# Kernel optimization log

Hardware: AMD Instinct MI355X
Metric: run time of the kernel (lower is better)

## Reference

```python
import jax, jax.numpy as jnp
import numpy as np

B, L, D = 2, 1536, 1024
H, P = 16, 1024
HD = P // H  # 64
K_SIZE = 5
DIFF_STEPS = 3
ALPHA = 0.02
NEG = -1e9
EPS = 1e-9


def setup_inputs() -> dict:
    key = jax.random.key(0)
    ks = jax.random.split(key, 12)
    s = 0.02
    hidden_states = jax.random.normal(ks[0], (B, L, D), dtype=jnp.float32)
    attention_mask = jax.random.randint(ks[1], (B, L), 0, 2, dtype=jnp.int32)
    Wq = jax.random.normal(ks[2], (D, P), dtype=jnp.float32) * s
    bq = jax.random.normal(ks[3], (P,), dtype=jnp.float32) * s
    Wk = jax.random.normal(ks[4], (D, P), dtype=jnp.float32) * s
    bk = jax.random.normal(ks[5], (P,), dtype=jnp.float32) * s
    Wv = jax.random.normal(ks[6], (D, P), dtype=jnp.float32) * s
    bv = jax.random.normal(ks[7], (P,), dtype=jnp.float32) * s
    Wo = jax.random.normal(ks[8], (P, D), dtype=jnp.float32) * s
    bo = jax.random.normal(ks[9], (D,), dtype=jnp.float32) * s
    kernel_w = jax.random.normal(ks[10], (K_SIZE,), dtype=jnp.float32)
    return {"hidden_states": hidden_states, "attention_mask": attention_mask,
            "Wq": Wq, "bq": bq, "Wk": Wk, "bk": bk, "Wv": Wv, "bv": bv,
            "Wo": Wo, "bo": bo, "kernel_w": kernel_w}


def _causal_smooth(p, w):
    # p: (B,H,Lq,Lk); causal cross-correlation matching F.conv1d(pad=k-1)[:Lk]
    k = w.shape[0]
    Lk = p.shape[-1]
    pp = jnp.pad(p, ((0, 0), (0, 0), (0, 0), (k - 1, 0)))
    out = w[0] * pp[..., 0:Lk]
    for j in range(1, k):
        out = out + w[j] * pp[..., j:j + Lk]
    return out


def reference(hidden_states, attention_mask, Wq, bq, Wk, bk, Wv, bv, Wo, bo, kernel_w):
    mask_f = attention_mask.astype(hidden_states.dtype)  # (B,Lk), 1=keep
    additive = (1.0 - mask_f) * NEG                       # (B,Lk)
    key_valid = (attention_mask > 0).astype(hidden_states.dtype)

    Q = (hidden_states @ Wq + bq).reshape(B, L, H, HD)
    Kt = (hidden_states @ Wk + bk).reshape(B, L, H, HD)
    V = (hidden_states @ Wv + bv).reshape(B, L, H, HD)

    scores = jnp.einsum('bqhd,bkhd->bhqk', Q, Kt) / np.sqrt(HD).astype(np.float32)
    scores = scores + additive[:, None, None, :]
    p = jax.nn.softmax(scores, axis=-1)  # (B,H,Lq,Lk)

    w = jax.nn.softmax(kernel_w)  # (k,)
    kv4 = key_valid[:, None, None, :]
    for _ in range(DIFF_STEPS):
        ps = _causal_smooth(p, w)
        ps = ps * kv4
        ps = ps / (jnp.sum(ps, axis=-1, keepdims=True) + EPS)
        p = (1.0 - ALPHA) * p + ALPHA * ps

    attn = jnp.einsum('bhqk,bkhd->bqhd', p, V).reshape(B, L, P)
    return attn @ Wo + bo
```

## Files before the change

kernel.cpp:

```cpp
#include <hip/hip_runtime.h>

#define BB 2
#define LL 1536
#define DD 1024
#define HH 16
#define HDD 64
#define PP 1024
#define PBS 1544

typedef __attribute__((ext_vector_type(8))) __bf16 bf16x8;
typedef __attribute__((ext_vector_type(4))) float f32x4;
typedef __attribute__((ext_vector_type(2))) float f32x2;

__device__ __forceinline__ float b2f(unsigned short u) {
  unsigned int x = ((unsigned int)u) << 16;
  return __builtin_bit_cast(float, x);
}
__device__ __forceinline__ unsigned short f2b(float f) {
  unsigned int x = __builtin_bit_cast(unsigned int, f);
  unsigned int r = (x + 0x7FFFu + ((x >> 16) & 1u)) >> 16;
  return (unsigned short)r;
}
__device__ __forceinline__ bf16x8 ldb8(const unsigned short* p) {
  return __builtin_bit_cast(bf16x8, *(const uint4*)p);
}
__device__ __forceinline__ f32x2 mk2(float a, float b) {
  f32x2 r;
  r.x = a;
  r.y = b;
  return r;
}
__device__ __forceinline__ void gl_lds16(const unsigned short* g,
                                         unsigned short* l) {
  __builtin_amdgcn_global_load_lds(
      (const __attribute__((address_space(1))) void*)g,
      (__attribute__((address_space(3))) void*)l, 16, 0, 0);
}

template <int CTRL>
__device__ __forceinline__ float dppadd(float x) {
  int s = __builtin_amdgcn_update_dpp(0, __builtin_bit_cast(int, x), CTRL, 0xf,
                                      0xf, true);
  return x + __builtin_bit_cast(float, s);
}
__device__ __forceinline__ float wave_sum64(float x) {
  x = dppadd<0x111>(x);
  x = dppadd<0x112>(x);
  x = dppadd<0x114>(x);
  x = dppadd<0x118>(x);
  x = dppadd<0x142>(x);
  x = dppadd<0x143>(x);
  return __builtin_bit_cast(
      float, __builtin_amdgcn_readlane(__builtin_bit_cast(int, x), 63));
}

__global__ __launch_bounds__(256) void prep(
    const float* __restrict__ hs, unsigned short* __restrict__ hsb,
    const float* __restrict__ Wq, const float* __restrict__ Wk,
    const float* __restrict__ Wv, const float* __restrict__ Wo,
    unsigned short* __restrict__ WT) {
  const int bid = blockIdx.x;
  const int t = threadIdx.x;
  if (bid < 1536) {
    const int idx = bid * 2048 + t * 8;
    float4 a = *(const float4*)(hs + idx);
    float4 b = *(const float4*)(hs + idx + 4);
    uint4 u;
    u.x = (unsigned int)f2b(a.x) | ((unsigned int)f2b(a.y) << 16);
    u.y = (unsigned int)f2b(a.z) | ((unsigned int)f2b(a.w) << 16);
    u.z = (unsigned int)f2b(b.x) | ((unsigned int)f2b(b.y) << 16);
    u.w = (unsigned int)f2b(b.z) | ((unsigned int)f2b(b.w) << 16);
    *(uint4*)(hsb + idx) = u;
  } else {
    __shared__ float tile[64][68];
    const int t2 = bid - 1536;
    const int z = t2 >> 8;
    const int bx = t2 & 15, by = (t2 >> 4) & 15;
    const float* W = (z == 0) ? Wq : (z == 1) ? Wk : (z == 2) ? Wv : Wo;
    unsigned short* O = WT + (size_t)z * 1024 * 1024;
    const int r0 = by * 64;
    const int c0 = bx * 64;
#pragma unroll
    for (int i = 0; i < 4; ++i) {
      const int row = (t >> 4) + i * 16;
      const int col = (t & 15) * 4;
      *(float4*)&tile[row][col] =
          *(const float4*)&W[(size_t)(r0 + row) * 1024 + c0 + col];
    }
    __syncthreads();
#pragma unroll
    for (int i = 0; i < 4; ++i) {
      const int n = (t >> 4) + i * 16;
      const int k4 = (t & 15) * 4;
      uint2 u;
      u.x = (unsigned int)f2b(tile[k4 + 0][n]) |
            ((unsigned int)f2b(tile[k4 + 1][n]) << 16);
      u.y = (unsigned int)f2b(tile[k4 + 2][n]) |
            ((unsigned int)f2b(tile[k4 + 3][n]) << 16);
      *(uint2*)&O[(size_t)(c0 + n) * 1024 + r0 + k4] = u;
    }
  }
}

template <int MODE>
__device__ __forceinline__ void gemm_mfma_body(
    const unsigned short* __restrict__ A, const unsigned short* __restrict__ Bt,
    const float* __restrict__ bias, void* __restrict__ Cout) {
  __shared__ unsigned short As[128 * 32];
  __shared__ unsigned short Bs[128 * 32];
  const int t = threadIdx.x;
  const int lane = t & 63;
  const int w = t >> 6;
  const int quad = lane >> 4;
  const int lc = lane & 15;
  const int m0 = blockIdx.y * 128, n0 = blockIdx.x * 128;

  const int sr = lane >> 2;
  const int sk = (lane & 3) * 8;
  const unsigned short* ga0 = A + (size_t)(m0 + w * 32 + sr) * 1024 + sk;
  const unsigned short* ga1 = ga0 + 16 * 1024;
  const unsigned short* gb0 = Bt + (size_t)(n0 + w * 32 + sr) * 1024 + sk;
  const unsigned short* gb1 = gb0 + 16 * 1024;
  unsigned short* la0 = As + w * 1024;
  unsigned short* la1 = As + w * 1024 + 512;
  unsigned short* lb0 = Bs + w * 1024;
  unsigned short* lb1 = Bs + w * 1024 + 512;

  const int mrow0 = (w >> 1) * 64, ncol0 = (w & 1) * 64;

  f32x4 acc[4][4];
#pragma unroll
  for (int i = 0; i < 4; ++i)
#pragma unroll
    for (int j = 0; j < 4; ++j) acc[i][j] = (f32x4){0.f, 0.f, 0.f, 0.f};

  for (int k0 = 0; k0 < 1024; k0 += 32) {
    __syncthreads();
    gl_lds16(ga0 + k0, la0);
    gl_lds16(ga1 + k0, la1);
    gl_lds16(gb0 + k0, lb0);
    gl_lds16(gb1 + k0, lb1);
    __syncthreads();
    bf16x8 af[4], bfr[4];
#pragma unroll
    for (int i = 0; i < 4; ++i)
      af[i] = ldb8(&As[(mrow0 + i * 16 + lc) * 32 + quad * 8]);
#pragma unroll
    for (int j = 0; j < 4; ++j)
      bfr[j] = ldb8(&Bs[(ncol0 + j * 16 + lc) * 32 + quad * 8]);
#pragma unroll
    for (int i = 0; i < 4; ++i)
#pragma unroll
      for (int j = 0; j < 4; ++j)
        acc[i][j] =
            __builtin_amdgcn_mfma_f32_16x16x32_bf16(af[i], bfr[j], acc[i][j], 0, 0, 0);
  }

#pragma unroll
  for (int i = 0; i < 4; ++i) {
    const int row0 = m0 + mrow0 + i * 16 + quad * 4;
#pragma unroll
    for (int jj = 0; jj < 4; ++jj) {
      const int col = n0 + ncol0 + jj * 16 + lc;
      const float bz = bias[col];
      float o[4];
#pragma unroll
      for (int r = 0; r < 4; ++r) o[r] = acc[i][jj][r] + bz;
      if constexpr (MODE == 0) {
        const int bb = row0 / LL;
        const int ql = row0 - bb * LL;
        const int qt = ql >> 4;
        const int m = ql & 15;
        const int hh = col >> 6;
        const int hd = col & 63;
        const int f = hd >> 5;
        const int qk = (hd >> 3) & 3;
        const int j = hd & 7;
        unsigned short* QF = (unsigned short*)Cout;
        const size_t base =
            (((size_t)(bb * HH + hh) * 96 + qt) * 2 + f) * 512 +
            (qk * 16 + m) * 8 + j;
#pragma unroll
        for (int r = 0; r < 4; ++r) QF[base + r * 8] = f2b(o[r] * 0.125f);
      } else if constexpr (MODE == 1) {
        const int bb = row0 / LL;
        const int kl = row0 - bb * LL;
        const int ktl = kl >> 4;
        const int m = kl & 15;
        const int hh = col >> 6;
        const int hd = col & 63;
        const int f = hd >> 5;
        const int qk = (hd >> 3) & 3;
        const int j = hd & 7;
        unsigned short* KF = (unsigned short*)Cout;
        const size_t base =
            (((size_t)(bb * HH + hh) * 96 + ktl) * 2 + f) * 512 +
            (qk * 16 + m) * 8 + j;
#pragma unroll
        for (int r = 0; r < 4; ++r) KF[base + r * 8] = f2b(o[r]);
      } else if constexpr (MODE == 2) {
        const int bb = row0 / LL;
        const int kl = row0 - bb * LL;
        const int hh = col >> 6;
        const int hd = col & 63;
        const int hg = hd >> 4;
        const int lcv = hd & 15;
        const int tile = (kl >> 5);
        const int qv = (kl >> 3) & 3;
        const int j0 = kl & 7;
        unsigned short* VF = (unsigned short*)Cout;
        const size_t base =
            (((size_t)(bb * HH + hh) * 4 + hg) * 48 + tile) * 512 +
            (qv * 16 + lcv) * 8 + j0;
        uint2 u;
        u.x = (unsigned int)f2b(o[0]) | ((unsigned int)f2b(o[1]) << 16);
        u.y = (unsigned int)f2b(o[2]) | ((unsigned int)f2b(o[3]) << 16);
        *(uint2*)&VF[base] = u;
      } else {
#pragma unroll
        for (int r = 0; r < 4; ++r)
          ((float*)Cout)[(size_t)(row0 + r) * 1024 + col] = o[r];
      }
    }
  }
}

__global__ __launch_bounds__(256) void qkv_gemm(
    const unsigned short* __restrict__ hsb, const unsigned short* __restrict__ WT,
    const float* __restrict__ bq, const float* __restrict__ bk,
    const float* __restrict__ bv, unsigned short* __restrict__ QF,
    unsigned short* __restrict__ KF, unsigned short* __restrict__ VF) {
  if (blockIdx.z == 0) {
    gemm_mfma_body<0>(hsb, WT, bq, QF);
  } else if (blockIdx.z == 1) {
    gemm_mfma_body<1>(hsb, WT + 1024 * 1024, bk, KF);
  } else {
    gemm_mfma_body<2>(hsb, WT + 2 * 1024 * 1024, bv, VF);
  }
}

__global__ __launch_bounds__(256) void out_gemm(
    const unsigned short* __restrict__ ctxb,
    const unsigned short* __restrict__ WoT, const float* __restrict__ bo,
    float* __restrict__ out) {
  gemm_mfma_body<3>(ctxb, WoT, bo, out);
}

__global__ __launch_bounds__(512, 4) void attn_kernel(
    const unsigned short* __restrict__ QF, const unsigned short* __restrict__ KF,
    const unsigned short* __restrict__ VF, const int* __restrict__ mask,
    const float* __restrict__ kernel_w, unsigned short* __restrict__ ctxb) {
  __shared__ __align__(16) unsigned short p_b[16][PBS];
  __shared__ unsigned int kvb[50];
  __shared__ float red_s[8][16];

  const int t = threadIdx.x;
  const int lane = t & 63;
  const int w = t >> 6;
  const int quad = lane >> 4;
  const int lc = lane & 15;
  const int b = blockIdx.z, h = blockIdx.y;
  const int q0 = blockIdx.x * 16;

  if (t < 2) kvb[48 + t] = 0;
#pragma unroll
  for (int r = 0; r < 3; ++r) {
    const int idx = r * 512 + t;
    unsigned long long bal = __ballot(mask[b * LL + idx] > 0);
    if (lane == 0) {
      const int base = (r * 512 + w * 64) >> 5;
      kvb[base] = (unsigned int)bal;
      kvb[base + 1] = (unsigned int)(bal >> 32);
    }
  }
  __syncthreads();

  const unsigned short* qfb =
      QF + (((size_t)(b * HH + h) * 96 + (q0 >> 4)) * 2) * 512 + lane * 8;
  const bf16x8 qb0 = ldb8(qfb);
  const bf16x8 qb1 = ldb8(qfb + 512);
  float sc[12][4];
  const unsigned short* kfb =
      KF + (((size_t)(b * HH + h) * 96 + w) * 2) * 512 + lane * 8;
#pragma unroll
  for (int j = 0; j < 12; ++j) {
    bf16x8 ka0 = ldb8(kfb + j * 8192);
    bf16x8 ka1 = ldb8(kfb + j * 8192 + 512);
    f32x4 acc = {0.f, 0.f, 0.f, 0.f};
    acc = __builtin_amdgcn_mfma_f32_16x16x32_bf16(ka0, qb0, acc, 0, 0, 0);
    acc = __builtin_amdgcn_mfma_f32_16x16x32_bf16(ka1, qb1, acc, 0, 0, 0);
    sc[j][0] = acc[0];
    sc[j][1] = acc[1];
    sc[j][2] = acc[2];
    sc[j][3] = acc[3];
  }

  const int kbase = w * 16 + quad * 4;
  const int gamma = kbase >> 5;
  const int beta = kbase & 31;
  float s = 0.f;
#pragma unroll
  for (int j = 0; j < 12; ++j) {
    const unsigned int w4 = (kvb[j * 4 + gamma] >> beta) & 0xFu;
#pragma unroll
    for (int r = 0; r < 4; ++r) {
      float e = ((w4 >> r) & 1u) ? __expf(sc[j][r]) : 0.f;
      sc[j][r] = e;
      s += e;
    }
  }
  s += __shfl_xor(s, 16, 64);
  s += __shfl_xor(s, 32, 64);
  if (lane < 16) red_s[w][lane] = s;
  __syncthreads();
  float tot0 = 0.f;
#pragma unroll
  for (int ww = 0; ww < 8; ++ww) tot0 += red_s[ww][lc];
  const float inv = 1.f / tot0;
#pragma unroll
  for (int j = 0; j < 12; ++j) {
    uint2 u;
    u.x = (unsigned int)f2b(sc[j][0] * inv) |
          ((unsigned int)f2b(sc[j][1] * inv) << 16);
    u.y = (unsigned int)f2b(sc[j][2] * inv) |
          ((unsigned int)f2b(sc[j][3] * inv) << 16);
    *(uint2*)&p_b[lc][j * 128 + kbase] = u;
  }
  __syncthreads();

  float wr[5];
  {
    float k0 = kernel_w[0], k1 = kernel_w[1], k2 = kernel_w[2],
          k3 = kernel_w[3], k4 = kernel_w[4];
    float km = fmaxf(fmaxf(fmaxf(k0, k1), fmaxf(k2, k3)), k4);
    float e0 = __expf(k0 - km), e1 = __expf(k1 - km), e2 = __expf(k2 - km),
          e3 = __expf(k3 - km), e4 = __expf(k4 - km);
    float es = e0 + e1 + e2 + e3 + e4;
    wr[0] = e4 / es;
    wr[1] = e3 / es;
    wr[2] = e2 / es;
    wr[3] = e1 / es;
    wr[4] = e0 / es;
  }
  unsigned int db;
  {
    const int w0i = (lane * 24) >> 5, sh = (lane * 24) & 31;
    unsigned long long kw2 =
        ((unsigned long long)kvb[w0i + 1] << 32) | (unsigned long long)kvb[w0i];
    db = (unsigned int)((kw2 >> sh) & 0xFFFFFFu);
  }
  f32x2 fm2[12];
#pragma unroll
  for (int i = 0; i < 12; ++i)
    fm2[i] = mk2((float)((db >> (2 * i)) & 1u), (float)((db >> (2 * i + 1)) & 1u));

  for (int rr = 0; rr < 2; ++rr) {
    const int row = w * 2 + rr;
    f32x2 pg[12];
#pragma unroll
    for (int c = 0; c < 3; ++c) {
      uint4 v = *(const uint4*)&p_b[row][lane * 24 + c * 8];
      unsigned int ws4[4] = {v.x, v.y, v.z, v.w};
#pragma unroll
      for (int q = 0; q < 4; ++q)
        pg[c * 4 + q] =
            mk2(__builtin_bit_cast(float, ws4[q] << 16),
                __builtin_bit_cast(float, ws4[q] & 0xFFFF0000u));
    }
#pragma unroll
    for (int step = 0; step < 3; ++step) {
      float h1 = __shfl_up(pg[11].y, 1);
      float h2 = __shfl_up(pg[11].x, 1);
      float h3 = __shfl_up(pg[10].y, 1);
      float h4 = __shfl_up(pg[10].x, 1);
      if (lane == 0) h1 = h2 = h3 = h4 = 0.f;
      f32x2 ps2[12];
      ps2[0] = wr[0] * pg[0] + wr[1] * mk2(h1, pg[0].x) + wr[2] * mk2(h2, h1) +
               wr[3] * mk2(h3, h2) + wr[4] * mk2(h4, h3);
      ps2[1] = wr[0] * pg[1] + wr[1] * mk2(pg[0].y, pg[1].x) + wr[2] * pg[0] +
               wr[3] * mk2(h1, pg[0].x) + wr[4] * mk2(h2, h1);
#pragma unroll
      for (int i = 2; i < 12; ++i)
        ps2[i] = wr[0] * pg[i] + wr[1] * mk2(pg[i - 1].y, pg[i].x) +
                 wr[2] * pg[i - 1] + wr[3] * mk2(pg[i - 2].y, pg[i - 1].x) +
                 wr[4] * pg[i - 2];
      f32x2 acc2 = mk2(0.f, 0.f);
#pragma unroll
      for (int i = 0; i < 12; ++i) {
        ps2[i] *= fm2[i];
        acc2 += ps2[i];
      }
      const float tot = wave_sum64(acc2.x + acc2.y);
      const float pinv = 0.02f / (tot + 1e-9f);
#pragma unroll
      for (int i = 0; i < 12; ++i) pg[i] = 0.98f * pg[i] + ps2[i] * pinv;
    }
#pragma unroll
    for (int c = 0; c < 3; ++c) {
      unsigned int uw[4];
#pragma unroll
      for (int q = 0; q < 4; ++q)
        uw[q] = (unsigned int)f2b(pg[c * 4 + q].x) |
                ((unsigned int)f2b(pg[c * 4 + q].y) << 16);
      uint4 u;
      u.x = uw[0];
      u.y = uw[1];
      u.z = uw[2];
      u.w = uw[3];
      *(uint4*)&p_b[row][lane * 24 + c * 8] = u;
    }
  }
  __syncthreads();

  const int cidx = (w & 3) * 16 + lc;
  const int gbase = (w >> 2) * 12;
  const unsigned short* vfb =
      VF + ((((size_t)(b * HH + h) * 4 + (w & 3)) * 48 + (w >> 2) * 24) * 512) +
      lane * 8;
  f32x4 oacc = {0.f, 0.f, 0.f, 0.f};
#pragma unroll
  for (int g = 0; g < 12; ++g) {
    const int gg = gbase + g;
#pragma unroll
    for (int c = 0; c < 2; ++c) {
      bf16x8 pa = ldb8(&p_b[lc][gg * 64 + c * 32 + quad * 8]);
      bf16x8 vf = ldb8(vfb + (g * 2 + c) * 512);
      oacc = __builtin_amdgcn_mfma_f32_16x16x32_bf16(pa, vf, oacc, 0, 0, 0);
    }
  }
  __syncthreads();
  float* pscr = (float*)&p_b[0][0];
  if (w >= 4) {
    const int idx = ((((w - 4) * 4 + quad) * 16) + lc) * 4;
    *(float4*)(pscr + idx) =
        make_float4(oacc[0], oacc[1], oacc[2], oacc[3]);
  }
  __syncthreads();
  if (w < 4) {
    const int idx = (((w * 4 + quad) * 16) + lc) * 4;
    float4 pr = *(const float4*)(pscr + idx);
    float o[4] = {oacc[0] + pr.x, oacc[1] + pr.y, oacc[2] + pr.z,
                  oacc[3] + pr.w};
#pragma unroll
    for (int r = 0; r < 4; ++r)
      ctxb[((size_t)(b * LL + q0 + quad * 4 + r)) * PP + h * HDD + cidx] =
          f2b(o[r]);
  }
}

extern "C" void kernel_launch(void* const* d_in, const int* in_sizes, int n_in,
                              void* d_out, int out_size, void* d_ws,
                              size_t ws_size, hipStream_t stream) {
  const float* hs = (const float*)d_in[0];
  const int* mask = (const int*)d_in[1];
  const float* Wq = (const float*)d_in[2];
  const float* bq = (const float*)d_in[3];
  const float* Wk = (const float*)d_in[4];
  const float* bk = (const float*)d_in[5];
  const float* Wv = (const float*)d_in[6];
  const float* bv = (const float*)d_in[7];
  const float* Wo = (const float*)d_in[8];
  const float* bo = (const float*)d_in[9];
  const float* kw = (const float*)d_in[10];

  const size_t NBLP = (size_t)BB * LL * PP;
  unsigned short* QF = (unsigned short*)d_ws;
  unsigned short* KF = QF + NBLP;
  unsigned short* VF = KF + NBLP;
  unsigned short* ctxb = VF + NBLP;
  unsigned short* hsb = ctxb + NBLP;
  unsigned short* WT = hsb + NBLP;

  dim3 blk(256);
  prep<<<dim3(2560), blk, 0, stream>>>(hs, hsb, Wq, Wk, Wv, Wo, WT);
  qkv_gemm<<<dim3(8, 24, 3), blk, 0, stream>>>(hsb, WT, bq, bk, bv, QF, KF, VF);
  attn_kernel<<<dim3(96, 16, 2), dim3(512), 0, stream>>>(QF, KF, VF, mask, kw,
                                                         ctxb);
  out_gemm<<<dim3(8, 24, 1), blk, 0, stream>>>(ctxb, WT + 3 * 1024 * 1024, bo,
                                               (float*)d_out);
}
```

Baseline: 242.1 us.

## Run causal smoothing diffusion as MFMA banded matmul over contiguous key ownership

Reworks the attention kernel so each wave owns a contiguous block of 192 keys. The 5-tap causal smoothing now runs as an MFMA against a banded Toeplitz weight matrix built from the softmaxed kernel, instead of per-lane FMA chains with shuffles. Probabilities stay in registers across diffusion steps. LDS holds them in a new fragment-friendly packed layout with a zero halo tile, and block-wide reductions use fdot2 on fp16-packed masked values. This cuts VALU work in the diffusion loop but adds block-level syncs per step, and the fp16/bf16 rounding of the smoothed values adds precision risk.

```diff
diff --git a/kernel.cpp b/kernel.cpp
--- a/kernel.cpp
+++ b/kernel.cpp
@@ -6,16 +6,12 @@
 #define HH 16
 #define HDD 64
 #define PP 1024
-#define PBS 1544
 
 typedef __attribute__((ext_vector_type(8))) __bf16 bf16x8;
 typedef __attribute__((ext_vector_type(4))) float f32x4;
 typedef __attribute__((ext_vector_type(2))) float f32x2;
-
-__device__ __forceinline__ float b2f(unsigned short u) {
-  unsigned int x = ((unsigned int)u) << 16;
-  return __builtin_bit_cast(float, x);
-}
+typedef _Float16 f16x2 __attribute__((ext_vector_type(2)));
+
 __device__ __forceinline__ unsigned short f2b(float f) {
   unsigned int x = __builtin_bit_cast(unsigned int, f);
   unsigned int r = (x + 0x7FFFu + ((x >> 16) & 1u)) >> 16;
@@ -30,28 +26,26 @@
   r.y = b;
   return r;
 }
+__device__ __forceinline__ unsigned int cvtpk_bf16(float lo, float hi) {
+  unsigned int r;
+  asm("v_cvt_pk_bf16_f32 %0, %1, %2" : "=v"(r) : "v"(lo), "v"(hi));
+  return r;
+}
+__device__ __forceinline__ float fdot2u(unsigned int a, unsigned int ones,
+                                        float c) {
+#if __has_builtin(__builtin_amdgcn_fdot2)
+  return __builtin_amdgcn_fdot2(__builtin_bit_cast(f16x2, a),
+                                __builtin_bit_cast(f16x2, ones), c, false);
+#else
+  f16x2 x = __builtin_bit_cast(f16x2, a);
+  return c + (float)x.x + (float)x.y;
+#endif
+}
 __device__ __forceinline__ void gl_lds16(const unsigned short* g,
                                          unsigned short* l) {
   __builtin_amdgcn_global_load_lds(
       (const __attribute__((address_space(1))) void*)g,
       (__attribute__((address_space(3))) void*)l, 16, 0, 0);
-}
-
-template <int CTRL>
-__device__ __forceinline__ float dppadd(float x) {
-  int s = __builtin_amdgcn_update_dpp(0, __builtin_bit_cast(int, x), CTRL, 0xf,
-                                      0xf, true);
-  return x + __builtin_bit_cast(float, s);
-}
-__device__ __forceinline__ float wave_sum64(float x) {
-  x = dppadd<0x111>(x);
-  x = dppadd<0x112>(x);
-  x = dppadd<0x114>(x);
-  x = dppadd<0x118>(x);
-  x = dppadd<0x142>(x);
-  x = dppadd<0x143>(x);
-  return __builtin_bit_cast(
-      float, __builtin_amdgcn_readlane(__builtin_bit_cast(int, x), 63));
 }
 
 __global__ __launch_bounds__(256) void prep(
@@ -152,8 +146,8 @@
     for (int i = 0; i < 4; ++i)
 #pragma unroll
       for (int j = 0; j < 4; ++j)
-        acc[i][j] =
-            __builtin_amdgcn_mfma_f32_16x16x32_bf16(af[i], bfr[j], acc[i][j], 0, 0, 0);
+        acc[i][j] = __builtin_amdgcn_mfma_f32_16x16x32_bf16(af[i], bfr[j],
+                                                            acc[i][j], 0, 0, 0);
   }
 
 #pragma unroll
@@ -177,9 +171,8 @@
         const int qk = (hd >> 3) & 3;
         const int j = hd & 7;
         unsigned short* QF = (unsigned short*)Cout;
-        const size_t base =
-            (((size_t)(bb * HH + hh) * 96 + qt) * 2 + f) * 512 +
-            (qk * 16 + m) * 8 + j;
+        const size_t base = (((size_t)(bb * HH + hh) * 96 + qt) * 2 + f) * 512 +
+                            (qk * 16 + m) * 8 + j;
 #pragma unroll
         for (int r = 0; r < 4; ++r) QF[base + r * 8] = f2b(o[r] * 0.125f);
       } else if constexpr (MODE == 1) {
@@ -209,9 +202,8 @@
         const int qv = (kl >> 3) & 3;
         const int j0 = kl & 7;
         unsigned short* VF = (unsigned short*)Cout;
-        const size_t base =
-            (((size_t)(bb * HH + hh) * 4 + hg) * 48 + tile) * 512 +
-            (qv * 16 + lcv) * 8 + j0;
+        const size_t base = (((size_t)(bb * HH + hh) * 4 + hg) * 48 + tile) * 512 +
+                            (qv * 16 + lcv) * 8 + j0;
         uint2 u;
         u.x = (unsigned int)f2b(o[0]) | ((unsigned int)f2b(o[1]) << 16);
         u.y = (unsigned int)f2b(o[2]) | ((unsigned int)f2b(o[3]) << 16);
@@ -226,10 +218,11 @@
 }
 
 __global__ __launch_bounds__(256) void qkv_gemm(
-    const unsigned short* __restrict__ hsb, const unsigned short* __restrict__ WT,
-    const float* __restrict__ bq, const float* __restrict__ bk,
-    const float* __restrict__ bv, unsigned short* __restrict__ QF,
-    unsigned short* __restrict__ KF, unsigned short* __restrict__ VF) {
+    const unsigned short* __restrict__ hsb,
+    const unsigned short* __restrict__ WT, const float* __restrict__ bq,
+    const float* __restrict__ bk, const float* __restrict__ bv,
+    unsigned short* __restrict__ QF, unsigned short* __restrict__ KF,
+    unsigned short* __restrict__ VF) {
   if (blockIdx.z == 0) {
     gemm_mfma_body<0>(hsb, WT, bq, QF);
   } else if (blockIdx.z == 1) {
@@ -247,12 +240,14 @@
 }
 
 __global__ __launch_bounds__(512, 4) void attn_kernel(
-    const unsigned short* __restrict__ QF, const unsigned short* __restrict__ KF,
+    const unsigned short* __restrict__ QF,
+    const unsigned short* __restrict__ KF,
     const unsigned short* __restrict__ VF, const int* __restrict__ mask,
     const float* __restrict__ kernel_w, unsigned short* __restrict__ ctxb) {
-  __shared__ __align__(16) unsigned short p_b[16][PBS];
-  __shared__ unsigned int kvb[50];
+  __shared__ __align__(16) unsigned int P2u[97 * 128];
+  __shared__ unsigned int kvb[48];
   __shared__ float red_s[8][16];
+  __shared__ float wext[48];
 
   const int t = threadIdx.x;
   const int lane = t & 63;
@@ -262,7 +257,6 @@
   const int b = blockIdx.z, h = blockIdx.y;
   const int q0 = blockIdx.x * 16;
 
-  if (t < 2) kvb[48 + t] = 0;
 #pragma unroll
   for (int r = 0; r < 3; ++r) {
     const int idx = r * 512 + t;
@@ -273,62 +267,7 @@
       kvb[base + 1] = (unsigned int)(bal >> 32);
     }
   }
-  __syncthreads();
-
-  const unsigned short* qfb =
-      QF + (((size_t)(b * HH + h) * 96 + (q0 >> 4)) * 2) * 512 + lane * 8;
-  const bf16x8 qb0 = ldb8(qfb);
-  const bf16x8 qb1 = ldb8(qfb + 512);
-  float sc[12][4];
-  const unsigned short* kfb =
-      KF + (((size_t)(b * HH + h) * 96 + w) * 2) * 512 + lane * 8;
-#pragma unroll
-  for (int j = 0; j < 12; ++j) {
-    bf16x8 ka0 = ldb8(kfb + j * 8192);
-    bf16x8 ka1 = ldb8(kfb + j * 8192 + 512);
-    f32x4 acc = {0.f, 0.f, 0.f, 0.f};
-    acc = __builtin_amdgcn_mfma_f32_16x16x32_bf16(ka0, qb0, acc, 0, 0, 0);
-    acc = __builtin_amdgcn_mfma_f32_16x16x32_bf16(ka1, qb1, acc, 0, 0, 0);
-    sc[j][0] = acc[0];
-    sc[j][1] = acc[1];
-    sc[j][2] = acc[2];
-    sc[j][3] = acc[3];
-  }
-
-  const int kbase = w * 16 + quad * 4;
-  const int gamma = kbase >> 5;
-  const int beta = kbase & 31;
-  float s = 0.f;
-#pragma unroll
-  for (int j = 0; j < 12; ++j) {
-    const unsigned int w4 = (kvb[j * 4 + gamma] >> beta) & 0xFu;
-#pragma unroll
-    for (int r = 0; r < 4; ++r) {
-      float e = ((w4 >> r) & 1u) ? __expf(sc[j][r]) : 0.f;
-      sc[j][r] = e;
-      s += e;
-    }
-  }
-  s += __shfl_xor(s, 16, 64);
-  s += __shfl_xor(s, 32, 64);
-  if (lane < 16) red_s[w][lane] = s;
-  __syncthreads();
-  float tot0 = 0.f;
-#pragma unroll
-  for (int ww = 0; ww < 8; ++ww) tot0 += red_s[ww][lc];
-  const float inv = 1.f / tot0;
-#pragma unroll
-  for (int j = 0; j < 12; ++j) {
-    uint2 u;
-    u.x = (unsigned int)f2b(sc[j][0] * inv) |
-          ((unsigned int)f2b(sc[j][1] * inv) << 16);
-    u.y = (unsigned int)f2b(sc[j][2] * inv) |
-          ((unsigned int)f2b(sc[j][3] * inv) << 16);
-    *(uint2*)&p_b[lc][j * 128 + kbase] = u;
-  }
-  __syncthreads();
-
-  float wr[5];
+  if (t < 128) P2u[t] = 0;
   {
     float k0 = kernel_w[0], k1 = kernel_w[1], k2 = kernel_w[2],
           k3 = kernel_w[3], k4 = kernel_w[4];
@@ -336,111 +275,161 @@
     float e0 = __expf(k0 - km), e1 = __expf(k1 - km), e2 = __expf(k2 - km),
           e3 = __expf(k3 - km), e4 = __expf(k4 - km);
     float es = e0 + e1 + e2 + e3 + e4;
-    wr[0] = e4 / es;
-    wr[1] = e3 / es;
-    wr[2] = e2 / es;
-    wr[3] = e1 / es;
-    wr[4] = e0 / es;
-  }
-  unsigned int db;
+    if (t < 48) {
+      float v = 0.f;
+      if (t == 16) v = e4 / es;
+      if (t == 17) v = e3 / es;
+      if (t == 18) v = e2 / es;
+      if (t == 19) v = e1 / es;
+      if (t == 20) v = e0 / es;
+      wext[t] = v;
+    }
+  }
+  __syncthreads();
+
+  bf16x8 afb;
   {
-    const int w0i = (lane * 24) >> 5, sh = (lane * 24) & 31;
-    unsigned long long kw2 =
-        ((unsigned long long)kvb[w0i + 1] << 32) | (unsigned long long)kvb[w0i];
-    db = (unsigned int)((kw2 >> sh) & 0xFFFFFFu);
-  }
-  f32x2 fm2[12];
-#pragma unroll
-  for (int i = 0; i < 12; ++i)
-    fm2[i] = mk2((float)((db >> (2 * i)) & 1u), (float)((db >> (2 * i + 1)) & 1u));
-
-  for (int rr = 0; rr < 2; ++rr) {
-    const int row = w * 2 + rr;
-    f32x2 pg[12];
-#pragma unroll
-    for (int c = 0; c < 3; ++c) {
-      uint4 v = *(const uint4*)&p_b[row][lane * 24 + c * 8];
-      unsigned int ws4[4] = {v.x, v.y, v.z, v.w};
-#pragma unroll
-      for (int q = 0; q < 4; ++q)
-        pg[c * 4 + q] =
-            mk2(__builtin_bit_cast(float, ws4[q] << 16),
-                __builtin_bit_cast(float, ws4[q] & 0xFFFF0000u));
-    }
-#pragma unroll
-    for (int step = 0; step < 3; ++step) {
-      float h1 = __shfl_up(pg[11].y, 1);
-      float h2 = __shfl_up(pg[11].x, 1);
-      float h3 = __shfl_up(pg[10].y, 1);
-      float h4 = __shfl_up(pg[10].x, 1);
-      if (lane == 0) h1 = h2 = h3 = h4 = 0.f;
-      f32x2 ps2[12];
-      ps2[0] = wr[0] * pg[0] + wr[1] * mk2(h1, pg[0].x) + wr[2] * mk2(h2, h1) +
-               wr[3] * mk2(h3, h2) + wr[4] * mk2(h4, h3);
-      ps2[1] = wr[0] * pg[1] + wr[1] * mk2(pg[0].y, pg[1].x) + wr[2] * pg[0] +
-               wr[3] * mk2(h1, pg[0].x) + wr[4] * mk2(h2, h1);
-#pragma unroll
-      for (int i = 2; i < 12; ++i)
-        ps2[i] = wr[0] * pg[i] + wr[1] * mk2(pg[i - 1].y, pg[i].x) +
-                 wr[2] * pg[i - 1] + wr[3] * mk2(pg[i - 2].y, pg[i - 1].x) +
-                 wr[4] * pg[i - 2];
-      f32x2 acc2 = mk2(0.f, 0.f);
-#pragma unroll
-      for (int i = 0; i < 12; ++i) {
-        ps2[i] *= fm2[i];
-        acc2 += ps2[i];
-      }
-      const float tot = wave_sum64(acc2.x + acc2.y);
-      const float pinv = 0.02f / (tot + 1e-9f);
-#pragma unroll
-      for (int i = 0; i < 12; ++i) pg[i] = 0.98f * pg[i] + ps2[i] * pinv;
-    }
-#pragma unroll
-    for (int c = 0; c < 3; ++c) {
-      unsigned int uw[4];
-#pragma unroll
-      for (int q = 0; q < 4; ++q)
-        uw[q] = (unsigned int)f2b(pg[c * 4 + q].x) |
-                ((unsigned int)f2b(pg[c * 4 + q].y) << 16);
-      uint4 u;
-      u.x = uw[0];
-      u.y = uw[1];
-      u.z = uw[2];
-      u.w = uw[3];
-      *(uint4*)&p_b[row][lane * 24 + c * 8] = u;
-    }
-  }
+    const int kb = lc + 32 - quad * 8;
+    float bv[8];
+#pragma unroll
+    for (int jj = 0; jj < 8; ++jj) bv[jj] = wext[kb - jj];
+    uint4 uu;
+    uu.x = cvtpk_bf16(bv[0], bv[1]);
+    uu.y = cvtpk_bf16(bv[2], bv[3]);
+    uu.z = cvtpk_bf16(bv[4], bv[5]);
+    uu.w = cvtpk_bf16(bv[6], bv[7]);
+    afb = __builtin_bit_cast(bf16x8, uu);
+  }
+
+  const unsigned short* qfb =
+      QF + (((size_t)(b * HH + h) * 96 + (q0 >> 4)) * 2) * 512 + lane * 8;
+  const bf16x8 qb0 = ldb8(qfb);
+  const bf16x8 qb1 = ldb8(qfb + 512);
+  const unsigned short* kfb =
+      KF + (((size_t)(b * HH + h) * 96 + 12 * w) * 2) * 512 + lane * 8;
+  f32x2 pr[24];
+#pragma unroll
+  for (int j = 0; j < 12; ++j) {
+    bf16x8 ka0 = ldb8(kfb + j * 1024);
+    bf16x8 ka1 = ldb8(kfb + j * 1024 + 512);
+    f32x4 acc = {0.f, 0.f, 0.f, 0.f};
+    acc = __builtin_amdgcn_mfma_f32_16x16x32_bf16(ka0, qb0, acc, 0, 0, 0);
+    acc = __builtin_amdgcn_mfma_f32_16x16x32_bf16(ka1, qb1, acc, 0, 0, 0);
+    pr[2 * j] = mk2(acc[0], acc[1]);
+    pr[2 * j + 1] = mk2(acc[2], acc[3]);
+  }
+
+  unsigned int m_and[24];
+  float s = 0.f;
+#pragma unroll
+  for (int j = 0; j < 12; ++j) {
+    const int kb16 = 16 * j + 4 * quad;
+    const unsigned int w4 = (kvb[6 * w + (kb16 >> 5)] >> (kb16 & 31)) & 0xFu;
+    float e0 = (w4 & 1u) ? __expf(pr[2 * j].x) : 0.f;
+    float e1 = (w4 & 2u) ? __expf(pr[2 * j].y) : 0.f;
+    float e2 = (w4 & 4u) ? __expf(pr[2 * j + 1].x) : 0.f;
+    float e3 = (w4 & 8u) ? __expf(pr[2 * j + 1].y) : 0.f;
+    pr[2 * j] = mk2(e0, e1);
+    pr[2 * j + 1] = mk2(e2, e3);
+    s += (e0 + e1) + (e2 + e3);
+    m_and[2 * j] = ((w4 & 1u) ? 0xFFFFu : 0u) | ((w4 & 2u) ? 0xFFFF0000u : 0u);
+    m_and[2 * j + 1] =
+        ((w4 & 4u) ? 0xFFFFu : 0u) | ((w4 & 8u) ? 0xFFFF0000u : 0u);
+  }
+  s += __shfl_xor(s, 16, 64);
+  s += __shfl_xor(s, 32, 64);
+  if (lane < 16) red_s[w][lane] = s;
   __syncthreads();
+  float tot0 = 0.f;
+#pragma unroll
+  for (int ww = 0; ww < 8; ++ww) tot0 += red_s[ww][lc];
+  const float inv = 1.f / tot0;
+#pragma unroll
+  for (int i = 0; i < 24; ++i) pr[i] = pr[i] * inv;
+
+  unsigned int* const pwb = &P2u[((12 * w + 1) * 16 + lc) * 8 + 2 * quad];
+#pragma unroll
+  for (int j = 0; j < 12; ++j) {
+    uint2 u;
+    u.x = cvtpk_bf16(pr[2 * j].x, pr[2 * j].y);
+    u.y = cvtpk_bf16(pr[2 * j + 1].x, pr[2 * j + 1].y);
+    *(uint2*)(pwb + j * 128) = u;
+  }
+  __syncthreads();
+
+  const unsigned int ones2 = 0x3C003C00u;
+  const unsigned int* const prb =
+      &P2u[((12 * w + (quad >> 1)) * 16 + lc) * 8 + (quad & 1) * 4];
+#pragma unroll
+  for (int step = 0; step < 3; ++step) {
+    unsigned int s_pk[24];
+    float sum = 0.f;
+#pragma unroll
+    for (int j = 0; j < 12; ++j) {
+      bf16x8 bfr = ldb8((const unsigned short*)(prb + j * 128));
+      f32x4 z = {0.f, 0.f, 0.f, 0.f};
+      f32x4 ps = __builtin_amdgcn_mfma_f32_16x16x32_bf16(afb, bfr, z, 0, 0, 0);
+      unsigned int h0 =
+          __builtin_bit_cast(unsigned int, __builtin_amdgcn_cvt_pkrtz(ps[0], ps[1]));
+      unsigned int h1 =
+          __builtin_bit_cast(unsigned int, __builtin_amdgcn_cvt_pkrtz(ps[2], ps[3]));
+      s_pk[2 * j] = h0 & m_and[2 * j];
+      s_pk[2 * j + 1] = h1 & m_and[2 * j + 1];
+      sum = fdot2u(s_pk[2 * j], ones2, sum);
+      sum = fdot2u(s_pk[2 * j + 1], ones2, sum);
+    }
+    sum += __shfl_xor(sum, 16, 64);
+    sum += __shfl_xor(sum, 32, 64);
+    if (lane < 16) red_s[w][lane] = sum;
+    __syncthreads();
+    float tot = 0.f;
+#pragma unroll
+    for (int ww = 0; ww < 8; ++ww) tot += red_s[ww][lc];
+    const float pinv = 0.02f / (tot + 1e-9f);
+#pragma unroll
+    for (int i = 0; i < 24; ++i) {
+      f16x2 hp = __builtin_bit_cast(f16x2, s_pk[i]);
+      pr[i] = pr[i] * 0.98f + mk2((float)hp.x, (float)hp.y) * pinv;
+    }
+#pragma unroll
+    for (int j = 0; j < 12; ++j) {
+      uint2 u;
+      u.x = cvtpk_bf16(pr[2 * j].x, pr[2 * j].y);
+      u.y = cvtpk_bf16(pr[2 * j + 1].x, pr[2 * j + 1].y);
+      *(uint2*)(pwb + j * 128) = u;
+    }
+    __syncthreads();
+  }
 
   const int cidx = (w & 3) * 16 + lc;
   const int gbase = (w >> 2) * 12;
   const unsigned short* vfb =
       VF + ((((size_t)(b * HH + h) * 4 + (w & 3)) * 48 + (w >> 2) * 24) * 512) +
       lane * 8;
+  const unsigned int* const pvb =
+      &P2u[((4 * gbase + (quad >> 1) + 1) * 16 + lc) * 8 + (quad & 1) * 4];
   f32x4 oacc = {0.f, 0.f, 0.f, 0.f};
 #pragma unroll
   for (int g = 0; g < 12; ++g) {
-    const int gg = gbase + g;
 #pragma unroll
     for (int c = 0; c < 2; ++c) {
-      bf16x8 pa = ldb8(&p_b[lc][gg * 64 + c * 32 + quad * 8]);
+      bf16x8 pa = ldb8((const unsigned short*)(pvb + (4 * g + 2 * c) * 128));
       bf16x8 vf = ldb8(vfb + (g * 2 + c) * 512);
       oacc = __builtin_amdgcn_mfma_f32_16x16x32_bf16(pa, vf, oacc, 0, 0, 0);
     }
   }
   __syncthreads();
-  float* pscr = (float*)&p_b[0][0];
+  float* pscr = (float*)&P2u[0];
   if (w >= 4) {
     const int idx = ((((w - 4) * 4 + quad) * 16) + lc) * 4;
-    *(float4*)(pscr + idx) =
-        make_float4(oacc[0], oacc[1], oacc[2], oacc[3]);
+    *(float4*)(pscr + idx) = make_float4(oacc[0], oacc[1], oacc[2], oacc[3]);
   }
   __syncthreads();
   if (w < 4) {
     const int idx = (((w * 4 + quad) * 16) + lc) * 4;
-    float4 pr = *(const float4*)(pscr + idx);
-    float o[4] = {oacc[0] + pr.x, oacc[1] + pr.y, oacc[2] + pr.z,
-                  oacc[3] + pr.w};
+    float4 prr = *(const float4*)(pscr + idx);
+    float o[4] = {oacc[0] + prr.x, oacc[1] + prr.y, oacc[2] + prr.z,
+                  oacc[3] + prr.w};
 #pragma unroll
     for (int r = 0; r < 4; ++r)
       ctxb[((size_t)(b * LL + q0 + quad * 4 + r)) * PP + h * HDD + cidx] =
```

Result: slower. 301.2 us (+24.4%).
